# Performance work log

Hardware: AMD Instinct MI355X
Metric: run time of the kernel (lower is better)

The kernel has to match this reference:

```python
import jax, jax.numpy as jnp
import numpy as np

B, T, D, H = 2, 2048, 1024, 16
DH = D // H  # 64


def setup_inputs() -> dict:
    key = jax.random.key(0)
    ks = jax.random.split(key, 6)
    s = 1.0 / np.sqrt(D)
    return {
        "x": jax.random.normal(ks[0], (B, T, D), dtype=jnp.float32),
        "Wq": jax.random.normal(ks[1], (D, D), dtype=jnp.float32) * s,
        "Wk": jax.random.normal(ks[2], (D, D), dtype=jnp.float32) * s,
        "Wv": jax.random.normal(ks[3], (D, D), dtype=jnp.float32) * s,
        "Wo": jax.random.normal(ks[4], (D, D), dtype=jnp.float32) * s,
        "bo": jnp.zeros((D,), dtype=jnp.float32),
    }


def reference(x, Wq, Wk, Wv, Wo, bo):
    b, t, _ = x.shape
    # projections (torch Linear: x @ W.T; here W stored as [d_in, d_out])
    q = (x @ Wq).reshape(b, t, H, DH).transpose(0, 2, 1, 3)  # [b,H,t,dh]
    k = (x @ Wk).reshape(b, t, H, DH).transpose(0, 2, 1, 3)
    v = (x @ Wv).reshape(b, t, H, DH).transpose(0, 2, 1, 3)
    scores = jnp.einsum("bhqd,bhkd->bhqk", q, k) / np.sqrt(DH).astype(np.float32)
    causal = jnp.tril(jnp.ones((t, t), dtype=bool))  # True = keep
    scores = jnp.where(causal, scores, -jnp.inf)
    weights = jax.nn.softmax(scores, axis=-1)
    ctx = jnp.einsum("bhqk,bhkd->bhqd", weights, v)
    ctx = ctx.transpose(0, 2, 1, 3).reshape(b, t, D)
    return ctx @ Wo + bo
```

## Files before the change

### kernel.cpp

```cpp
#include <hip/hip_runtime.h>


typedef unsigned short u16;
typedef __attribute__((ext_vector_type(8))) short short8;
typedef __attribute__((ext_vector_type(4))) short short4_t;
typedef __attribute__((ext_vector_type(4))) float f32x4;

#define B_ 2
#define T_ 2048
#define D_ 1024
#define H_ 16
#define DH_ 64
#define M_ (B_ * T_)
#define SCALE_LOG2E 0.18033688011112042f
#define NEG_BIG -3.0e4f

#define SLOT_F 4160
#define SLOTS_PER_BH 72
#define OPART_BYTES ((size_t)32 * SLOTS_PER_BH * SLOT_F * 4)
#define WS_BASE_BYTES ((size_t)24 * 1024 * 1024 * 2)

#define GLOAD16(g, l)                                                     \
  __builtin_amdgcn_global_load_lds(                                       \
      (const __attribute__((address_space(1))) void*)(g),                 \
      (__attribute__((address_space(3))) void*)(l), 16, 0, 0)

__device__ __forceinline__ u16 f2bf(float f) {
  union { float f; unsigned u; } v; v.f = f;
  unsigned r = v.u + 0x7fffu + ((v.u >> 16) & 1u);
  return (u16)(r >> 16);
}
__device__ __forceinline__ u16 f2bf_trunc(float f) {
  union { float f; unsigned u; } v; v.f = f;
  return (u16)(v.u >> 16);
}
__device__ __forceinline__ float exp2_raw(float x) {
  float r;
  asm volatile("v_exp_f32 %0, %1" : "=v"(r) : "v"(x));
  return r;
}

__global__ __launch_bounds__(256) void prep(
    const float* __restrict__ x, const float* __restrict__ w0,
    const float* __restrict__ w1, const float* __restrict__ w2,
    const float* __restrict__ w3, u16* __restrict__ xb,
    u16* __restrict__ outT) {
  __shared__ u16 Tl[64][72];
  const int id = blockIdx.x;
  const int tid = threadIdx.x;

  if (id < 2048) {
    const int i = (id * 256 + tid) * 8;
    float4 a = *(const float4*)(x + i);
    float4 b = *(const float4*)(x + i + 4);
    short8 o;
    o[0] = (short)f2bf(a.x); o[1] = (short)f2bf(a.y);
    o[2] = (short)f2bf(a.z); o[3] = (short)f2bf(a.w);
    o[4] = (short)f2bf(b.x); o[5] = (short)f2bf(b.y);
    o[6] = (short)f2bf(b.z); o[7] = (short)f2bf(b.w);
    *(short8*)(xb + i) = o;
    return;
  }

  const int id2 = id - 2048;
  const int z = id2 >> 8;
  const int rem = id2 & 255;
  const int r0 = (rem >> 4) * 64, c0 = (rem & 15) * 64;
  const float* src = (z == 0) ? w0 : (z == 1) ? w1 : (z == 2) ? w2 : w3;
  const int rr = tid >> 2, cc = (tid & 3) * 16;

  const float* p = src + (size_t)(r0 + rr) * D_ + c0 + cc;
  float4 f0 = *(const float4*)p;
  float4 f1 = *(const float4*)(p + 4);
  float4 f2 = *(const float4*)(p + 8);
  float4 f3 = *(const float4*)(p + 12);
  Tl[rr][cc + 0] = f2bf(f0.x); Tl[rr][cc + 1] = f2bf(f0.y);
  Tl[rr][cc + 2] = f2bf(f0.z); Tl[rr][cc + 3] = f2bf(f0.w);
  Tl[rr][cc + 4] = f2bf(f1.x); Tl[rr][cc + 5] = f2bf(f1.y);
  Tl[rr][cc + 6] = f2bf(f1.z); Tl[rr][cc + 7] = f2bf(f1.w);
  Tl[rr][cc + 8] = f2bf(f2.x); Tl[rr][cc + 9] = f2bf(f2.y);
  Tl[rr][cc +10] = f2bf(f2.z); Tl[rr][cc +11] = f2bf(f2.w);
  Tl[rr][cc +12] = f2bf(f3.x); Tl[rr][cc +13] = f2bf(f3.y);
  Tl[rr][cc +14] = f2bf(f3.z); Tl[rr][cc +15] = f2bf(f3.w);
  __syncthreads();

  u16* o = outT + (size_t)z * D_ * D_ + (size_t)(c0 + rr) * D_ + r0 + cc;
  short8 x0, x1;
#pragma unroll
  for (int i = 0; i < 8; i++) x0[i] = (short)Tl[cc + i][rr];
#pragma unroll
  for (int i = 0; i < 8; i++) x1[i] = (short)Tl[cc + 8 + i][rr];
  *(short8*)o = x0;
  *(short8*)(o + 8) = x1;
}

__global__ __launch_bounds__(256) void qkv_gemm(
    const u16* __restrict__ x, const u16* __restrict__ wT,
    u16* __restrict__ qkv) {
  __shared__ u16 As[128][32];
  __shared__ u16 Bs[128][32];

  const int n0 = blockIdx.x * 128;
  const int z = n0 >> 10;
  const int m0 = blockIdx.y * 128;
  const int tid = threadIdx.x;
  const int lane = tid & 63, w = tid >> 6;
  const int quad = lane >> 4, l16 = lane & 15;
  const int wr = w >> 1, wc = w & 1;

  f32x4 acc[4][4] = {};
  const int grow = w * 16 + (lane >> 2);
  const int gcol = (lane & 3) * 8;
  u16* lA = (u16*)As + w * 512;
  u16* lB = (u16*)Bs + w * 512;

  for (int k0 = 0; k0 < D_; k0 += 32) {
    const u16* gA = x + (size_t)(m0 + grow) * D_ + k0 + gcol;
    const u16* gB = wT + (size_t)(n0 + grow) * D_ + k0 + gcol;
    GLOAD16(gA, lA);
    GLOAD16(gA + (size_t)64 * D_, lA + 2048);
    GLOAD16(gB, lB);
    GLOAD16(gB + (size_t)64 * D_, lB + 2048);
    __syncthreads();

    short8 af[4], bf[4];
#pragma unroll
    for (int i = 0; i < 4; i++)
      af[i] = *(const short8*)&As[wr * 64 + i * 16 + l16][quad * 8];
#pragma unroll
    for (int i = 0; i < 4; i++)
      bf[i] = *(const short8*)&Bs[wc * 64 + i * 16 + l16][quad * 8];
#pragma unroll
    for (int i = 0; i < 4; i++)
#pragma unroll
      for (int j = 0; j < 4; j++)
        acc[i][j] = __builtin_amdgcn_mfma_f32_16x16x32_bf16(af[i], bf[j], acc[i][j], 0, 0, 0);
    __syncthreads();
  }

  if (z < 2) {
    u16* out = qkv + (size_t)z * M_ * D_;
    const float osc = (z == 0) ? SCALE_LOG2E : 1.0f;
#pragma unroll
    for (int i = 0; i < 4; i++) {
#pragma unroll
      for (int j = 0; j < 4; j++) {
        const int n = n0 + wc * 64 + j * 16 + l16;
        const int h = (n >> 6) & 15, dh = n & 63;
#pragma unroll
        for (int r = 0; r < 4; r++) {
          const int m = m0 + wr * 64 + i * 16 + quad * 4 + r;
          const int b = m >> 11, t = m & (T_ - 1);
          out[(((size_t)(b * H_ + h)) * T_ + t) * DH_ + dh] = f2bf(acc[i][j][r] * osc);
        }
      }
    }
  } else {
    u16* vt = qkv + (size_t)2 * M_ * D_;
#pragma unroll
    for (int i = 0; i < 4; i++) {
      const int mm = m0 + wr * 64 + i * 16 + quad * 4;
      const int b = mm >> 11, t = mm & (T_ - 1);
#pragma unroll
      for (int j = 0; j < 4; j++) {
        const int n = n0 + wc * 64 + j * 16 + l16;
        const int h = (n >> 6) & 15, dh = n & 63;
        short4_t pk;
#pragma unroll
        for (int r = 0; r < 4; r++) pk[r] = (short)f2bf(acc[i][j][r]);
        *(short4_t*)(vt + ((size_t)(b * H_ + h) * DH_ + dh) * T_ + t) = pk;
      }
    }
  }
}

__device__ __forceinline__ int slot_base(int qt) {
  return (qt < 16) ? (qt - 8) * 2
       : (qt < 24) ? 16 + (qt - 16) * 3
                   : 40 + (qt - 24) * 4;
}

__global__ __launch_bounds__(128) void attn_chunk(
    const u16* __restrict__ qg, const u16* __restrict__ kg,
    const u16* __restrict__ vtg, u16* __restrict__ ctx,
    float* __restrict__ Opart) {
  __shared__ u16 Ks[64][72];
  __shared__ u16 Vs[64][72];
  __shared__ u16 Ps[2][2][16][72];

  const int cid = 79 - blockIdx.x;
  int qt, c, nc;
  if (cid < 8)       { qt = cid;                    c = 0;               nc = 1; }
  else if (cid < 24) { qt = 8  + ((cid - 8) >> 1);  c = (cid - 8) & 1;   nc = 2; }
  else if (cid < 48) { qt = 16 + (cid - 24) / 3;    c = (cid - 24) % 3;  nc = 3; }
  else               { qt = 24 + ((cid - 48) >> 2); c = (cid - 48) & 3;  nc = 4; }
  const int nt = qt + 1;
  const int kv_lo = (c * nt / nc) * 64;
  const int kv_hi = ((c + 1) * nt / nc) * 64;
  const int q0 = qt * 64;

  const int bh = blockIdx.y;
  const int tid = threadIdx.x;
  const int w = tid >> 6, lane = tid & 63;
  const int quad = lane >> 4, l16 = lane & 15;
  const size_t baseQK = (size_t)bh * T_ * DH_;
  const size_t baseV  = (size_t)bh * DH_ * T_;

  const int qrowA = q0 + w * 32 + l16;
  const int qrowB = qrowA + 16;
  short8 qfA0 = *(const short8*)(qg + baseQK + (size_t)qrowA * DH_ + quad * 8);
  short8 qfA1 = *(const short8*)(qg + baseQK + (size_t)qrowA * DH_ + 32 + quad * 8);
  short8 qfB0 = *(const short8*)(qg + baseQK + (size_t)qrowB * DH_ + quad * 8);
  short8 qfB1 = *(const short8*)(qg + baseQK + (size_t)qrowB * DH_ + 32 + quad * 8);

  f32x4 oaccA[4] = {}, oaccB[4] = {};
  float liA = 0.f, liB = 0.f;

  const int srow = tid >> 1;
  const int scol = (tid & 1) * 32;

  const u16* kp = kg + baseQK + (size_t)(kv_lo + srow) * DH_ + scol;
  const u16* vp = vtg + baseV + (size_t)srow * T_ + kv_lo + scol;
  short8 kr0 = *(const short8*)kp;
  short8 kr1 = *(const short8*)(kp + 8);
  short8 kr2 = *(const short8*)(kp + 16);
  short8 kr3 = *(const short8*)(kp + 24);
  short8 vr0 = *(const short8*)vp;
  short8 vr1 = *(const short8*)(vp + 8);
  short8 vr2 = *(const short8*)(vp + 16);
  short8 vr3 = *(const short8*)(vp + 24);

  for (int kv0 = kv_lo; kv0 < kv_hi; kv0 += 64) {
    __syncthreads();
    *(short8*)&Ks[srow][scol]      = kr0;
    *(short8*)&Ks[srow][scol + 8]  = kr1;
    *(short8*)&Ks[srow][scol + 16] = kr2;
    *(short8*)&Ks[srow][scol + 24] = kr3;
    *(short8*)&Vs[srow][scol]      = vr0;
    *(short8*)&Vs[srow][scol + 8]  = vr1;
    *(short8*)&Vs[srow][scol + 16] = vr2;
    *(short8*)&Vs[srow][scol + 24] = vr3;
    __syncthreads();

    if (kv0 + 64 < kv_hi) {
      const u16* kn = kg + baseQK + (size_t)(kv0 + 64 + srow) * DH_ + scol;
      const u16* vn = vtg + baseV + (size_t)srow * T_ + kv0 + 64 + scol;
      kr0 = *(const short8*)kn;
      kr1 = *(const short8*)(kn + 8);
      kr2 = *(const short8*)(kn + 16);
      kr3 = *(const short8*)(kn + 24);
      vr0 = *(const short8*)vn;
      vr1 = *(const short8*)(vn + 8);
      vr2 = *(const short8*)(vn + 16);
      vr3 = *(const short8*)(vn + 24);
    }

    short8 kf0[4], kf1[4];
#pragma unroll
    for (int cb = 0; cb < 4; cb++) {
      kf0[cb] = *(const short8*)&Ks[cb * 16 + l16][quad * 8];
      kf1[cb] = *(const short8*)&Ks[cb * 16 + l16][32 + quad * 8];
    }

    f32x4 svA[4], svB[4];
    __builtin_amdgcn_s_setprio(1);
#pragma unroll
    for (int cb = 0; cb < 4; cb++) {
      f32x4 z = {};
      svA[cb] = __builtin_amdgcn_mfma_f32_16x16x32_bf16(kf0[cb], qfA0, z, 0, 0, 0);
      svA[cb] = __builtin_amdgcn_mfma_f32_16x16x32_bf16(kf1[cb], qfA1, svA[cb], 0, 0, 0);
      svB[cb] = __builtin_amdgcn_mfma_f32_16x16x32_bf16(kf0[cb], qfB0, z, 0, 0, 0);
      svB[cb] = __builtin_amdgcn_mfma_f32_16x16x32_bf16(kf1[cb], qfB1, svB[cb], 0, 0, 0);
    }
    __builtin_amdgcn_s_setprio(0);

    float pA[4][4], pB[4][4];
    if (kv0 == q0) {
#pragma unroll
      for (int cb = 0; cb < 4; cb++)
#pragma unroll
        for (int r = 0; r < 4; r++) {
          const int kv = kv0 + cb * 16 + quad * 4 + r;
          pA[cb][r] = exp2_raw((kv <= qrowA) ? svA[cb][r] : NEG_BIG);
          pB[cb][r] = exp2_raw((kv <= qrowB) ? svB[cb][r] : NEG_BIG);
        }
    } else {
#pragma unroll
      for (int cb = 0; cb < 4; cb++)
#pragma unroll
        for (int r = 0; r < 4; r++) {
          pA[cb][r] = exp2_raw(svA[cb][r]);
          pB[cb][r] = exp2_raw(svB[cb][r]);
        }
    }
#pragma unroll
    for (int cb = 0; cb < 4; cb++)
#pragma unroll
      for (int r = 0; r < 4; r++) { liA += pA[cb][r]; liB += pB[cb][r]; }

    short8 vf0[4], vf1[4];
#pragma unroll
    for (int cb = 0; cb < 4; cb++) {
      vf0[cb] = *(const short8*)&Vs[cb * 16 + l16][quad * 8];
      vf1[cb] = *(const short8*)&Vs[cb * 16 + l16][32 + quad * 8];
    }

#pragma unroll
    for (int cb = 0; cb < 4; cb++) {
      short4_t pkA, pkB;
#pragma unroll
      for (int r = 0; r < 4; r++) {
        pkA[r] = (short)f2bf_trunc(pA[cb][r]);
        pkB[r] = (short)f2bf_trunc(pB[cb][r]);
      }
      *(short4_t*)&Ps[w][0][l16][cb * 16 + quad * 4] = pkA;
      *(short4_t*)&Ps[w][1][l16][cb * 16 + quad * 4] = pkB;
    }
    short8 paA0 = *(const short8*)&Ps[w][0][l16][quad * 8];
    short8 paA1 = *(const short8*)&Ps[w][0][l16][32 + quad * 8];
    short8 paB0 = *(const short8*)&Ps[w][1][l16][quad * 8];
    short8 paB1 = *(const short8*)&Ps[w][1][l16][32 + quad * 8];
    __builtin_amdgcn_s_setprio(1);
#pragma unroll
    for (int cb = 0; cb < 4; cb++) {
      oaccA[cb] = __builtin_amdgcn_mfma_f32_16x16x32_bf16(vf0[cb], paA0, oaccA[cb], 0, 0, 0);
      oaccA[cb] = __builtin_amdgcn_mfma_f32_16x16x32_bf16(vf1[cb], paA1, oaccA[cb], 0, 0, 0);
      oaccB[cb] = __builtin_amdgcn_mfma_f32_16x16x32_bf16(vf0[cb], paB0, oaccB[cb], 0, 0, 0);
      oaccB[cb] = __builtin_amdgcn_mfma_f32_16x16x32_bf16(vf1[cb], paB1, oaccB[cb], 0, 0, 0);
    }
    __builtin_amdgcn_s_setprio(0);
  }

  liA += __shfl_xor(liA, 16, 64); liA += __shfl_xor(liA, 32, 64);
  liB += __shfl_xor(liB, 16, 64); liB += __shfl_xor(liB, 32, 64);

  if (nc == 1) {
    const int b = bh >> 4, h = bh & 15;
    const float invA = 1.0f / liA, invB = 1.0f / liB;
    u16* outA = ctx + ((size_t)(b * T_ + qrowA)) * D_ + h * 64 + quad * 4;
    u16* outB = ctx + ((size_t)(b * T_ + qrowB)) * D_ + h * 64 + quad * 4;
#pragma unroll
    for (int cb = 0; cb < 4; cb++) {
      short4_t oA, oB;
#pragma unroll
      for (int r = 0; r < 4; r++) {
        oA[r] = (short)f2bf(oaccA[cb][r] * invA);
        oB[r] = (short)f2bf(oaccB[cb][r] * invB);
      }
      *(short4_t*)(outA + cb * 16) = oA;
      *(short4_t*)(outB + cb * 16) = oB;
    }
  } else {
    float* slot = Opart + ((size_t)bh * SLOTS_PER_BH + slot_base(qt) + c) * SLOT_F;
    float* pA = slot + (size_t)(w * 32 + l16) * 64 + quad * 4;
    float* pB = slot + (size_t)(w * 32 + 16 + l16) * 64 + quad * 4;
#pragma unroll
    for (int cb = 0; cb < 4; cb++) {
      *(f32x4*)(pA + cb * 16) = oaccA[cb];
      *(f32x4*)(pB + cb * 16) = oaccB[cb];
    }
    if (quad == 0) {
      slot[4096 + w * 32 + l16] = liA;
      slot[4096 + w * 32 + 16 + l16] = liB;
    }
  }
}

__global__ __launch_bounds__(256) void attn_combine(
    const float* __restrict__ Opart, u16* __restrict__ ctx) {
  __shared__ float ls[64];
  const int qt = blockIdx.x + 8;
  const int bh = blockIdx.y;
  const int nc = 1 + (qt >> 3);
  const float* slot0 = Opart + ((size_t)bh * SLOTS_PER_BH + slot_base(qt)) * SLOT_F;
  const int tid = threadIdx.x;

  if (tid < 64) {
    float s = 0.f;
    for (int c = 0; c < nc; c++) s += slot0[(size_t)c * SLOT_F + 4096 + tid];
    ls[tid] = 1.0f / s;
  }
  __syncthreads();

  const int q = tid >> 2, d0 = (tid & 3) * 16;
  const float* p = slot0 + (size_t)q * 64 + d0;
  f32x4 a0 = *(const f32x4*)(p);
  f32x4 a1 = *(const f32x4*)(p + 4);
  f32x4 a2 = *(const f32x4*)(p + 8);
  f32x4 a3 = *(const f32x4*)(p + 12);
  for (int c = 1; c < nc; c++) {
    const float* pc = p + (size_t)c * SLOT_F;
    a0 += *(const f32x4*)(pc);
    a1 += *(const f32x4*)(pc + 4);
    a2 += *(const f32x4*)(pc + 8);
    a3 += *(const f32x4*)(pc + 12);
  }
  const float inv = ls[q];
  short8 o0, o1;
#pragma unroll
  for (int i = 0; i < 4; i++) {
    o0[i]     = (short)f2bf(a0[i] * inv);
    o0[i + 4] = (short)f2bf(a1[i] * inv);
    o1[i]     = (short)f2bf(a2[i] * inv);
    o1[i + 4] = (short)f2bf(a3[i] * inv);
  }
  const int b = bh >> 4, h = bh & 15;
  u16* op = ctx + ((size_t)(b * T_ + qt * 64 + q)) * D_ + h * 64 + d0;
  *(short8*)op = o0;
  *(short8*)(op + 8) = o1;
}

__global__ __launch_bounds__(128) void attn_mono(
    const u16* __restrict__ qg, const u16* __restrict__ kg,
    const u16* __restrict__ vtg, u16* __restrict__ ctx) {
  __shared__ u16 Ks[64][72];
  __shared__ u16 Vs[64][72];
  __shared__ u16 Ps[2][2][16][72];

  const int qt = gridDim.x - 1 - blockIdx.x;
  const int bh = blockIdx.y;
  const int tid = threadIdx.x;
  const int w = tid >> 6, lane = tid & 63;
  const int quad = lane >> 4, l16 = lane & 15;
  const int q0 = qt * 64;
  const size_t baseQK = (size_t)bh * T_ * DH_;
  const size_t baseV  = (size_t)bh * DH_ * T_;

  const int qrowA = q0 + w * 32 + l16;
  const int qrowB = qrowA + 16;
  short8 qfA0 = *(const short8*)(qg + baseQK + (size_t)qrowA * DH_ + quad * 8);
  short8 qfA1 = *(const short8*)(qg + baseQK + (size_t)qrowA * DH_ + 32 + quad * 8);
  short8 qfB0 = *(const short8*)(qg + baseQK + (size_t)qrowB * DH_ + quad * 8);
  short8 qfB1 = *(const short8*)(qg + baseQK + (size_t)qrowB * DH_ + 32 + quad * 8);

  f32x4 oaccA[4] = {}, oaccB[4] = {};
  float liA = 0.f, liB = 0.f;

  const int srow = tid >> 1;
  const int scol = (tid & 1) * 32;

  const u16* kp = kg + baseQK + (size_t)srow * DH_ + scol;
  const u16* vp = vtg + baseV + (size_t)srow * T_ + scol;
  short8 kr0 = *(const short8*)kp;
  short8 kr1 = *(const short8*)(kp + 8);
  short8 kr2 = *(const short8*)(kp + 16);
  short8 kr3 = *(const short8*)(kp + 24);
  short8 vr0 = *(const short8*)vp;
  short8 vr1 = *(const short8*)(vp + 8);
  short8 vr2 = *(const short8*)(vp + 16);
  short8 vr3 = *(const short8*)(vp + 24);

  for (int kv0 = 0; kv0 <= q0; kv0 += 64) {
    __syncthreads();
    *(short8*)&Ks[srow][scol]      = kr0;
    *(short8*)&Ks[srow][scol + 8]  = kr1;
    *(short8*)&Ks[srow][scol + 16] = kr2;
    *(short8*)&Ks[srow][scol + 24] = kr3;
    *(short8*)&Vs[srow][scol]      = vr0;
    *(short8*)&Vs[srow][scol + 8]  = vr1;
    *(short8*)&Vs[srow][scol + 16] = vr2;
    *(short8*)&Vs[srow][scol + 24] = vr3;
    __syncthreads();
    if (kv0 < q0) {
      const u16* kn = kg + baseQK + (size_t)(kv0 + 64 + srow) * DH_ + scol;
      const u16* vn = vtg + baseV + (size_t)srow * T_ + kv0 + 64 + scol;
      kr0 = *(const short8*)kn;
      kr1 = *(const short8*)(kn + 8);
      kr2 = *(const short8*)(kn + 16);
      kr3 = *(const short8*)(kn + 24);
      vr0 = *(const short8*)vn;
      vr1 = *(const short8*)(vn + 8);
      vr2 = *(const short8*)(vn + 16);
      vr3 = *(const short8*)(vn + 24);
    }

    short8 kf0[4], kf1[4];
#pragma unroll
    for (int cb = 0; cb < 4; cb++) {
      kf0[cb] = *(const short8*)&Ks[cb * 16 + l16][quad * 8];
      kf1[cb] = *(const short8*)&Ks[cb * 16 + l16][32 + quad * 8];
    }

    f32x4 svA[4], svB[4];
#pragma unroll
    for (int cb = 0; cb < 4; cb++) {
      f32x4 z = {};
      svA[cb] = __builtin_amdgcn_mfma_f32_16x16x32_bf16(kf0[cb], qfA0, z, 0, 0, 0);
      svA[cb] = __builtin_amdgcn_mfma_f32_16x16x32_bf16(kf1[cb], qfA1, svA[cb], 0, 0, 0);
      svB[cb] = __builtin_amdgcn_mfma_f32_16x16x32_bf16(kf0[cb], qfB0, z, 0, 0, 0);
      svB[cb] = __builtin_amdgcn_mfma_f32_16x16x32_bf16(kf1[cb], qfB1, svB[cb], 0, 0, 0);
    }

    float pA[4][4], pB[4][4];
    if (kv0 == q0) {
#pragma unroll
      for (int cb = 0; cb < 4; cb++)
#pragma unroll
        for (int r = 0; r < 4; r++) {
          const int kv = kv0 + cb * 16 + quad * 4 + r;
          pA[cb][r] = exp2_raw((kv <= qrowA) ? svA[cb][r] : NEG_BIG);
          pB[cb][r] = exp2_raw((kv <= qrowB) ? svB[cb][r] : NEG_BIG);
        }
    } else {
#pragma unroll
      for (int cb = 0; cb < 4; cb++)
#pragma unroll
        for (int r = 0; r < 4; r++) {
          pA[cb][r] = exp2_raw(svA[cb][r]);
          pB[cb][r] = exp2_raw(svB[cb][r]);
        }
    }
#pragma unroll
    for (int cb = 0; cb < 4; cb++)
#pragma unroll
      for (int r = 0; r < 4; r++) { liA += pA[cb][r]; liB += pB[cb][r]; }

    short8 vf0[4], vf1[4];
#pragma unroll
    for (int cb = 0; cb < 4; cb++) {
      vf0[cb] = *(const short8*)&Vs[cb * 16 + l16][quad * 8];
      vf1[cb] = *(const short8*)&Vs[cb * 16 + l16][32 + quad * 8];
    }

#pragma unroll
    for (int cb = 0; cb < 4; cb++) {
      short4_t pkA, pkB;
#pragma unroll
      for (int r = 0; r < 4; r++) {
        pkA[r] = (short)f2bf_trunc(pA[cb][r]);
        pkB[r] = (short)f2bf_trunc(pB[cb][r]);
      }
      *(short4_t*)&Ps[w][0][l16][cb * 16 + quad * 4] = pkA;
      *(short4_t*)&Ps[w][1][l16][cb * 16 + quad * 4] = pkB;
    }
    short8 paA0 = *(const short8*)&Ps[w][0][l16][quad * 8];
    short8 paA1 = *(const short8*)&Ps[w][0][l16][32 + quad * 8];
    short8 paB0 = *(const short8*)&Ps[w][1][l16][quad * 8];
    short8 paB1 = *(const short8*)&Ps[w][1][l16][32 + quad * 8];
#pragma unroll
    for (int cb = 0; cb < 4; cb++) {
      oaccA[cb] = __builtin_amdgcn_mfma_f32_16x16x32_bf16(vf0[cb], paA0, oaccA[cb], 0, 0, 0);
      oaccA[cb] = __builtin_amdgcn_mfma_f32_16x16x32_bf16(vf1[cb], paA1, oaccA[cb], 0, 0, 0);
      oaccB[cb] = __builtin_amdgcn_mfma_f32_16x16x32_bf16(vf0[cb], paB0, oaccB[cb], 0, 0, 0);
      oaccB[cb] = __builtin_amdgcn_mfma_f32_16x16x32_bf16(vf1[cb], paB1, oaccB[cb], 0, 0, 0);
    }
  }

  liA += __shfl_xor(liA, 16, 64); liA += __shfl_xor(liA, 32, 64);
  liB += __shfl_xor(liB, 16, 64); liB += __shfl_xor(liB, 32, 64);
  const int b = bh >> 4, h = bh & 15;
  const float invA = 1.0f / liA, invB = 1.0f / liB;
  u16* outA = ctx + ((size_t)(b * T_ + qrowA)) * D_ + h * 64 + quad * 4;
  u16* outB = ctx + ((size_t)(b * T_ + qrowB)) * D_ + h * 64 + quad * 4;
#pragma unroll
  for (int cb = 0; cb < 4; cb++) {
    short4_t oA, oB;
#pragma unroll
    for (int r = 0; r < 4; r++) {
      oA[r] = (short)f2bf(oaccA[cb][r] * invA);
      oB[r] = (short)f2bf(oaccB[cb][r] * invB);
    }
    *(short4_t*)(outA + cb * 16) = oA;
    *(short4_t*)(outB + cb * 16) = oB;
  }
}

__global__ __launch_bounds__(256) void out_gemm(
    const u16* __restrict__ ctx, const u16* __restrict__ woT,
    const float* __restrict__ bo, float* __restrict__ out) {
  __shared__ u16 As[64][32];
  __shared__ u16 Bs[128][32];

  const int n0 = blockIdx.x * 128;
  const int m0 = blockIdx.y * 64;
  const int tid = threadIdx.x;
  const int lane = tid & 63, w = tid >> 6;
  const int quad = lane >> 4, l16 = lane & 15;
  const int wr = w >> 1, wc = w & 1;

  f32x4 acc[2][4] = {};
  const int grow = w * 16 + (lane >> 2);
  const int gcol = (lane & 3) * 8;
  u16* lA = (u16*)As + w * 512;
  u16* lB = (u16*)Bs + w * 512;

  for (int k0 = 0; k0 < D_; k0 += 32) {
    const u16* gA = ctx + (size_t)(m0 + grow) * D_ + k0 + gcol;
    const u16* gB = woT + (size_t)(n0 + grow) * D_ + k0 + gcol;
    GLOAD16(gA, lA);
    GLOAD16(gB, lB);
    GLOAD16(gB + (size_t)64 * D_, lB + 2048);
    __syncthreads();

    short8 af[2], bf[4];
#pragma unroll
    for (int i = 0; i < 2; i++)
      af[i] = *(const short8*)&As[wr * 32 + i * 16 + l16][quad * 8];
#pragma unroll
    for (int i = 0; i < 4; i++)
      bf[i] = *(const short8*)&Bs[wc * 64 + i * 16 + l16][quad * 8];
#pragma unroll
    for (int i = 0; i < 2; i++)
#pragma unroll
      for (int j = 0; j < 4; j++)
        acc[i][j] = __builtin_amdgcn_mfma_f32_16x16x32_bf16(af[i], bf[j], acc[i][j], 0, 0, 0);
    __syncthreads();
  }

#pragma unroll
  for (int i = 0; i < 2; i++) {
#pragma unroll
    for (int j = 0; j < 4; j++) {
      const int n = n0 + wc * 64 + j * 16 + l16;
      const float bias = bo[n];
#pragma unroll
      for (int r = 0; r < 4; r++) {
        const int m = m0 + wr * 32 + i * 16 + quad * 4 + r;
        out[(size_t)m * D_ + n] = acc[i][j][r] + bias;
      }
    }
  }
}

extern "C" void kernel_launch(void* const* d_in, const int* in_sizes, int n_in,
                              void* d_out, int out_size, void* d_ws, size_t ws_size,
                              hipStream_t stream) {
  const float* x  = (const float*)d_in[0];
  const float* Wq = (const float*)d_in[1];
  const float* Wk = (const float*)d_in[2];
  const float* Wv = (const float*)d_in[3];
  const float* Wo = (const float*)d_in[4];
  const float* bo = (const float*)d_in[5];
  float* out = (float*)d_out;

  u16* ws  = (u16*)d_ws;
  u16* xb  = ws;
  u16* wT  = xb + (size_t)M_ * D_;
  u16* qkv = wT + (size_t)4 * D_ * D_;
  u16* ctx = qkv + (size_t)3 * M_ * D_;
  u16* vT  = qkv + (size_t)2 * M_ * D_;
  float* Opart = (float*)(ctx + (size_t)M_ * D_);

  prep<<<dim3(3072), 256, 0, stream>>>(x, Wq, Wk, Wv, Wo, xb, wT);
  qkv_gemm<<<dim3(24, 32), 256, 0, stream>>>(xb, wT, qkv);

  if (ws_size >= WS_BASE_BYTES + OPART_BYTES) {
    attn_chunk<<<dim3(80, B_ * H_), 128, 0, stream>>>(
        qkv, qkv + (size_t)M_ * D_, vT, ctx, Opart);
    attn_combine<<<dim3(24, B_ * H_), 256, 0, stream>>>(Opart, ctx);
  } else {
    attn_mono<<<dim3(T_ / 64, B_ * H_), 128, 0, stream>>>(
        qkv, qkv + (size_t)M_ * D_, vT, ctx);
  }

  out_gemm<<<dim3(D_ / 128, M_ / 64), 256, 0, stream>>>(ctx, wT + (size_t)3 * D_ * D_, bo, out);
}
```

Baseline: 205.6 us.

## Double-buffer LDS tiles in QKV and output projection GEMMs

Both projection GEMMs now keep two LDS buffers and issue the global-to-LDS loads for the next K slice before running the MFMAs on the current one. This lets the load of tile k+1 overlap the math on tile k, and drops one barrier per iteration. MFMA sections are also bracketed with s_setprio raises. It doubles the LDS footprint per block, which may reduce occupancy. Correctness relies on the compiler waiting on the async LDS loads before the barrier.

```diff
diff --git a/kernel.cpp b/kernel.cpp
--- a/kernel.cpp
+++ b/kernel.cpp
@@ -97,8 +97,8 @@
 __global__ __launch_bounds__(256) void qkv_gemm(
     const u16* __restrict__ x, const u16* __restrict__ wT,
     u16* __restrict__ qkv) {
-  __shared__ u16 As[128][32];
-  __shared__ u16 Bs[128][32];
+  __shared__ u16 As[2][128][32];
+  __shared__ u16 Bs[2][128][32];
 
   const int n0 = blockIdx.x * 128;
   const int z = n0 >> 10;
@@ -111,31 +111,50 @@
   f32x4 acc[4][4] = {};
   const int grow = w * 16 + (lane >> 2);
   const int gcol = (lane & 3) * 8;
-  u16* lA = (u16*)As + w * 512;
-  u16* lB = (u16*)Bs + w * 512;
-
+  const u16* gAr = x + (size_t)(m0 + grow) * D_ + gcol;
+  const u16* gBr = wT + (size_t)(n0 + grow) * D_ + gcol;
+  const int woff = w * 512;
+
+  {
+    u16* lA = (u16*)As + woff;
+    u16* lB = (u16*)Bs + woff;
+    GLOAD16(gAr, lA);
+    GLOAD16(gAr + (size_t)64 * D_, lA + 2048);
+    GLOAD16(gBr, lB);
+    GLOAD16(gBr + (size_t)64 * D_, lB + 2048);
+  }
+  __syncthreads();
+
+  int cur = 0;
   for (int k0 = 0; k0 < D_; k0 += 32) {
-    const u16* gA = x + (size_t)(m0 + grow) * D_ + k0 + gcol;
-    const u16* gB = wT + (size_t)(n0 + grow) * D_ + k0 + gcol;
-    GLOAD16(gA, lA);
-    GLOAD16(gA + (size_t)64 * D_, lA + 2048);
-    GLOAD16(gB, lB);
-    GLOAD16(gB + (size_t)64 * D_, lB + 2048);
-    __syncthreads();
+    if (k0 + 32 < D_) {
+      u16* lA = (u16*)As + (cur ^ 1) * 4096 + woff;
+      u16* lB = (u16*)Bs + (cur ^ 1) * 4096 + woff;
+      const u16* gA = gAr + k0 + 32;
+      const u16* gB = gBr + k0 + 32;
+      GLOAD16(gA, lA);
+      GLOAD16(gA + (size_t)64 * D_, lA + 2048);
+      GLOAD16(gB, lB);
+      GLOAD16(gB + (size_t)64 * D_, lB + 2048);
+    }
 
     short8 af[4], bf[4];
 #pragma unroll
     for (int i = 0; i < 4; i++)
-      af[i] = *(const short8*)&As[wr * 64 + i * 16 + l16][quad * 8];
+      af[i] = *(const short8*)&As[cur][wr * 64 + i * 16 + l16][quad * 8];
 #pragma unroll
     for (int i = 0; i < 4; i++)
-      bf[i] = *(const short8*)&Bs[wc * 64 + i * 16 + l16][quad * 8];
+      bf[i] = *(const short8*)&Bs[cur][wc * 64 + i * 16 + l16][quad * 8];
+    __builtin_amdgcn_s_setprio(1);
 #pragma unroll
     for (int i = 0; i < 4; i++)
 #pragma unroll
       for (int j = 0; j < 4; j++)
         acc[i][j] = __builtin_amdgcn_mfma_f32_16x16x32_bf16(af[i], bf[j], acc[i][j], 0, 0, 0);
+    __builtin_amdgcn_s_setprio(0);
+
     __syncthreads();
+    cur ^= 1;
   }
 
   if (z < 2) {
@@ -568,8 +587,8 @@
 __global__ __launch_bounds__(256) void out_gemm(
     const u16* __restrict__ ctx, const u16* __restrict__ woT,
     const float* __restrict__ bo, float* __restrict__ out) {
-  __shared__ u16 As[64][32];
-  __shared__ u16 Bs[128][32];
+  __shared__ u16 As[2][64][32];
+  __shared__ u16 Bs[2][128][32];
 
   const int n0 = blockIdx.x * 128;
   const int m0 = blockIdx.y * 64;
@@ -581,30 +600,48 @@
   f32x4 acc[2][4] = {};
   const int grow = w * 16 + (lane >> 2);
   const int gcol = (lane & 3) * 8;
-  u16* lA = (u16*)As + w * 512;
-  u16* lB = (u16*)Bs + w * 512;
-
+  const u16* gAr = ctx + (size_t)(m0 + grow) * D_ + gcol;
+  const u16* gBr = woT + (size_t)(n0 + grow) * D_ + gcol;
+  const int woff = w * 512;
+
+  {
+    u16* lA = (u16*)As + woff;
+    u16* lB = (u16*)Bs + woff;
+    GLOAD16(gAr, lA);
+    GLOAD16(gBr, lB);
+    GLOAD16(gBr + (size_t)64 * D_, lB + 2048);
+  }
+  __syncthreads();
+
+  int cur = 0;
   for (int k0 = 0; k0 < D_; k0 += 32) {
-    const u16* gA = ctx + (size_t)(m0 + grow) * D_ + k0 + gcol;
-    const u16* gB = woT + (size_t)(n0 + grow) * D_ + k0 + gcol;
-    GLOAD16(gA, lA);
-    GLOAD16(gB, lB);
-    GLOAD16(gB + (size_t)64 * D_, lB + 2048);
-    __syncthreads();
+    if (k0 + 32 < D_) {
+      u16* lA = (u16*)As + (cur ^ 1) * 2048 + woff;
+      u16* lB = (u16*)Bs + (cur ^ 1) * 4096 + woff;
+      const u16* gA = gAr + k0 + 32;
+      const u16* gB = gBr + k0 + 32;
+      GLOAD16(gA, lA);
+      GLOAD16(gB, lB);
+      GLOAD16(gB + (size_t)64 * D_, lB + 2048);
+    }
 
     short8 af[2], bf[4];
 #pragma unroll
     for (int i = 0; i < 2; i++)
-      af[i] = *(const short8*)&As[wr * 32 + i * 16 + l16][quad * 8];
+      af[i] = *(const short8*)&As[cur][wr * 32 + i * 16 + l16][quad * 8];
 #pragma unroll
     for (int i = 0; i < 4; i++)
-      bf[i] = *(const short8*)&Bs[wc * 64 + i * 16 + l16][quad * 8];
+      bf[i] = *(const short8*)&Bs[cur][wc * 64 + i * 16 + l16][quad * 8];
+    __builtin_amdgcn_s_setprio(1);
 #pragma unroll
     for (int i = 0; i < 2; i++)
 #pragma unroll
       for (int j = 0; j < 4; j++)
         acc[i][j] = __builtin_amdgcn_mfma_f32_16x16x32_bf16(af[i], bf[j], acc[i][j], 0, 0, 0);
+    __builtin_amdgcn_s_setprio(0);
+
     __syncthreads();
+    cur ^= 1;
   }
 
 #pragma unroll
```

New measurement: 189.9 us. 1.08x faster.
